# Kernel tuning notes

Hardware: AMD Instinct MI355X
Metric: run time of the kernel (lower is better)

Reference implementation:

```python
import jax, jax.numpy as jnp
import numpy as np

D = 1024
DK = 1024
B, S = 4, 2048

def setup_inputs() -> dict:
    key = jax.random.key(0)
    ks = jax.random.split(key, 7)
    x = jax.random.normal(ks[0], (B, S, D), dtype=jnp.float32)
    mask = jnp.zeros((B, S, S), dtype=jnp.float32)
    scale = 1.0 / np.sqrt(D)
    Wq = jax.random.normal(ks[1], (D, DK), dtype=jnp.float32) * scale
    bq = jax.random.normal(ks[2], (DK,), dtype=jnp.float32) * 0.01
    Wk = jax.random.normal(ks[3], (D, DK), dtype=jnp.float32) * scale
    bk = jax.random.normal(ks[4], (DK,), dtype=jnp.float32) * 0.01
    Wv = jax.random.normal(ks[5], (D, DK), dtype=jnp.float32) * scale
    bv = jax.random.normal(ks[6], (DK,), dtype=jnp.float32) * 0.01
    return {"x": x, "mask": mask, "Wq": Wq, "bq": bq, "Wk": Wk, "bk": bk, "Wv": Wv, "bv": bv}

def reference(x, mask, Wq, bq, Wk, bk, Wv, bv):
    # Q/K/V projections: [B,S,D] @ [D,DK] + bias -> [B,S,DK]
    Q = jnp.einsum('bsd,dk->bsk', x, Wq) + bq
    K = jnp.einsum('bsd,dk->bsk', x, Wk) + bk
    V = jnp.einsum('bsd,dk->bsk', x, Wv) + bv
    scale = 1.0 / jnp.sqrt(jnp.asarray(DK, dtype=Q.dtype))
    scores = jnp.einsum('bqk,bpk->bqp', Q, K) * scale + mask  # [B,S,S]
    attn = jax.nn.softmax(scores, axis=-1)
    return jnp.einsum('bqp,bpk->bqk', attn, V)
```

## Files before the change

### kernel.cpp

```cpp
#include <hip/hip_runtime.h>
#include <hip/hip_bf16.h>
#include <stdint.h>

typedef unsigned short u16;
typedef __attribute__((ext_vector_type(4))) unsigned short u16x4;
typedef __attribute__((ext_vector_type(8))) short short8;
typedef __attribute__((ext_vector_type(4))) float f32x4;

__device__ inline u16 f2b(float f) {
  uint32_t u = __builtin_bit_cast(uint32_t, f);
  u += 0x7fffu + ((u >> 16) & 1u);
  return (u16)(u >> 16);
}
__device__ inline float b2f(u16 b) {
  return __builtin_bit_cast(float, (uint32_t)b << 16);
}

__global__ __launch_bounds__(256) void cvt_f32_bf16(const float* __restrict__ in,
                                                    u16* __restrict__ out, long n) {
  long i = ((long)blockIdx.x * blockDim.x + threadIdx.x) * 4;
  if (i + 3 < n) {
    float4 v = *(const float4*)(in + i);
    u16x4 o = { f2b(v.x), f2b(v.y), f2b(v.z), f2b(v.w) };
    *(u16x4*)(out + i) = o;
  }
}

__global__ __launch_bounds__(256) void transpose_cvt3(const float* __restrict__ Wq,
                                                      const float* __restrict__ Wk,
                                                      const float* __restrict__ Wv,
                                                      u16* __restrict__ out) {
  const int z = blockIdx.z;
  const float* in = z == 0 ? Wq : (z == 1 ? Wk : Wv);
  u16* o = out + (long)z * 1024 * 1024;
  __shared__ float tile[32][33];
  int c0 = blockIdx.x * 32, r0 = blockIdx.y * 32;
#pragma unroll
  for (int j = 0; j < 32; j += 8)
    tile[threadIdx.y + j][threadIdx.x] = in[(long)(r0 + threadIdx.y + j) * 1024 + c0 + threadIdx.x];
  __syncthreads();
#pragma unroll
  for (int j = 0; j < 32; j += 8)
    o[(long)(c0 + threadIdx.y + j) * 1024 + r0 + threadIdx.x] = f2b(tile[threadIdx.x][threadIdx.y + j]);
}

__global__ __launch_bounds__(256) void concat_bias(const float* __restrict__ bq,
                                                   const float* __restrict__ bk,
                                                   const float* __restrict__ bv,
                                                   float* __restrict__ out) {
  int i = blockIdx.x * 256 + threadIdx.x;
  if (i < 3072)
    out[i] = i < 1024 ? bq[i] : (i < 2048 ? bk[i - 1024] : bv[i - 2048]);
}

#define BM 128
#define BN 128
#define BK 64

__device__ inline void load_lds16(const void* g, void* l) {
  __builtin_amdgcn_global_load_lds((const __attribute__((address_space(1))) void*)g,
                                   (__attribute__((address_space(3))) void*)l, 16, 0, 0);
}

__global__ __launch_bounds__(256, 2) void gemm_bt(
    const u16* __restrict__ A, const u16* __restrict__ Bt, void* __restrict__ C,
    u16* __restrict__ vtOut,
    const float* __restrict__ bias, const float* __restrict__ linv,
    int K, int lda, int ldb, int ldc,
    long sA, long sB, long sC,
    float scale, int mode)
{
  const int z = blockIdx.z;
  A += z * sA;
  Bt += z * sB;
  const long cbase = z * sC;
  const float* lz = linv ? linv + (long)z * 2048 : nullptr;

  __shared__ __align__(16) u16 lA[BM * BK];
  __shared__ __align__(16) u16 lB[BN * BK];

  const int t = threadIdx.x;
  const int lane = t & 63;
  const int wave = t >> 6;
  const int wr = wave >> 1, wc = wave & 1;
  const int m0 = blockIdx.y * BM, n0 = blockIdx.x * BN;

  const int srow = t >> 3;
  const int schunk = (t & 7) ^ (srow & 7);
  const u16* aS = A + (long)(m0 + srow) * lda + schunk * 8;
  const u16* bS = Bt + (long)(n0 + srow) * ldb + schunk * 8;

  f32x4 acc[4][4] = {};
  const int fr = lane & 15;
  const int q4 = lane >> 4;

  for (int k0 = 0; k0 < K; k0 += BK) {
    __syncthreads();
#pragma unroll
    for (int i = 0; i < 4; i++) {
      load_lds16(aS + k0 + (long)(i * 32) * lda, &lA[(i * 256 + t) * 8]);
      load_lds16(bS + k0 + (long)(i * 32) * ldb, &lB[(i * 256 + t) * 8]);
    }
    __syncthreads();
#pragma unroll
    for (int kk = 0; kk < 2; kk++) {
      const int ch = kk * 4 + q4;
      short8 aF[4], bF[4];
#pragma unroll
      for (int i = 0; i < 4; i++) {
        int row = wr * 64 + i * 16 + fr;
        aF[i] = *(const short8*)&lA[row * BK + ((ch ^ (row & 7)) * 8)];
      }
#pragma unroll
      for (int j = 0; j < 4; j++) {
        int row = wc * 64 + j * 16 + fr;
        bF[j] = *(const short8*)&lB[row * BK + ((ch ^ (row & 7)) * 8)];
      }
#pragma unroll
      for (int i = 0; i < 4; i++)
#pragma unroll
        for (int j = 0; j < 4; j++)
          acc[i][j] = __builtin_amdgcn_mfma_f32_16x16x32_bf16(aF[i], bF[j], acc[i][j], 0, 0, 0);
    }
  }

  const int r0 = q4 * 4;
#pragma unroll
  for (int i = 0; i < 4; i++) {
#pragma unroll
    for (int j = 0; j < 4; j++) {
      const int row = m0 + wr * 64 + i * 16 + r0;
      const int col = n0 + wc * 64 + j * 16 + fr;
      if (mode == 0) {
        const float b = bias[col];
        if (col >= 2048) {
          u16x4 o = { f2b(acc[i][j][0] + b), f2b(acc[i][j][1] + b),
                      f2b(acc[i][j][2] + b), f2b(acc[i][j][3] + b) };
          *(u16x4*)(vtOut + (long)(col - 2048) * 8192 + row) = o;
        } else {
#pragma unroll
          for (int r = 0; r < 4; r++)
            ((u16*)C)[(long)(row + r) * ldc + col] = f2b(acc[i][j][r] + b);
        }
      } else if (mode == 2) {
#pragma unroll
        for (int r = 0; r < 4; r++)
          ((u16*)C)[cbase + (long)(row + r) * ldc + col] = f2b(__expf(acc[i][j][r] * scale));
      } else {
#pragma unroll
        for (int r = 0; r < 4; r++)
          ((float*)C)[cbase + (long)(row + r) * ldc + col] = acc[i][j][r] * lz[row + r];
      }
    }
  }
}

__global__ __launch_bounds__(256) void maskexp_rows(u16* __restrict__ P,
                                                    const float* __restrict__ mask,
                                                    float* __restrict__ linv) {
  const long row = blockIdx.x;
  u16* p = P + row * 2048;
  const float* mk = mask + row * 2048;
  const int t = threadIdx.x;
  const int wave = t >> 6;

  u16x4 a0 = *(const u16x4*)(p + 8 * t);
  u16x4 a1 = *(const u16x4*)(p + 8 * t + 4);
  float4 m0 = *(const float4*)(mk + 8 * t);
  float4 m1 = *(const float4*)(mk + 8 * t + 4);

  float e[8];
  e[0] = b2f(a0.x) * __expf(m0.x); e[1] = b2f(a0.y) * __expf(m0.y);
  e[2] = b2f(a0.z) * __expf(m0.z); e[3] = b2f(a0.w) * __expf(m0.w);
  e[4] = b2f(a1.x) * __expf(m1.x); e[5] = b2f(a1.y) * __expf(m1.y);
  e[6] = b2f(a1.z) * __expf(m1.z); e[7] = b2f(a1.w) * __expf(m1.w);

  float sum = ((e[0] + e[1]) + (e[2] + e[3])) + ((e[4] + e[5]) + (e[6] + e[7]));
#pragma unroll
  for (int off = 32; off > 0; off >>= 1) sum += __shfl_xor(sum, off);
  __shared__ float reds[4];
  if ((t & 63) == 0) reds[wave] = sum;
  __syncthreads();
  sum = (reds[0] + reds[1]) + (reds[2] + reds[3]);
  if (t == 0) linv[row] = 1.0f / sum;

  u16x4 o0 = { f2b(e[0]), f2b(e[1]), f2b(e[2]), f2b(e[3]) };
  u16x4 o1 = { f2b(e[4]), f2b(e[5]), f2b(e[6]), f2b(e[7]) };
  *(u16x4*)(p + 8 * t) = o0;
  *(u16x4*)(p + 8 * t + 4) = o1;
}

extern "C" void kernel_launch(void* const* d_in, const int* in_sizes, int n_in,
                              void* d_out, int out_size, void* d_ws, size_t ws_size,
                              hipStream_t stream) {
  const float* x    = (const float*)d_in[0];
  const float* mask = (const float*)d_in[1];
  const float* Wq   = (const float*)d_in[2];
  const float* bq   = (const float*)d_in[3];
  const float* Wk   = (const float*)d_in[4];
  const float* bk   = (const float*)d_in[5];
  const float* Wv   = (const float*)d_in[6];
  const float* bv   = (const float*)d_in[7];
  float* out = (float*)d_out;

  char* w = (char*)d_ws;
  u16*   xb    = (u16*)(w);
  u16*   wT    = (u16*)(w + 16777216);
  float* biasC = (float*)(w + 23068672);
  u16*   QKV   = (u16*)(w + 23081088);
  u16*   Vt    = (u16*)(w + 73414016);
  u16*   Pp    = (u16*)(w + 90191232);
  float* linv  = (float*)(w + 123745664);

  cvt_f32_bf16<<<8192, 256, 0, stream>>>(x, xb, 8192L * 1024);
  transpose_cvt3<<<dim3(32, 32, 3), dim3(32, 8), 0, stream>>>(Wq, Wk, Wv, wT);
  concat_bias<<<12, 256, 0, stream>>>(bq, bk, bv, biasC);

  gemm_bt<<<dim3(24, 64, 1), 256, 0, stream>>>(xb, wT, QKV, Vt, biasC, nullptr,
      1024, 1024, 1024, 3072, 0, 0, 0, 1.0f, 0);

  gemm_bt<<<dim3(16, 16, 4), 256, 0, stream>>>(QKV, QKV + 1024, Pp, nullptr, nullptr, nullptr,
      1024, 3072, 3072, 2048,
      2048L * 3072, 2048L * 3072, 2048L * 2048, 0.03125f, 2);

  maskexp_rows<<<8192, 256, 0, stream>>>(Pp, mask, linv);

  gemm_bt<<<dim3(8, 16, 4), 256, 0, stream>>>(Pp, Vt, out, nullptr, nullptr, linv,
      2048, 2048, 8192, 1024,
      2048L * 2048, 2048L, 2048L * 1024, 1.0f, 4);
}
```

Before: 309.9 us.

## Fuse mask-exp and row-sum into the QK^T GEMM epilogue

Drops the separate maskexp_rows pass. The scores GEMM epilogue now stages exp(scores) through LDS, multiplies by exp(mask), writes P once with coalesced stores and accumulates partial row sums with atomicAdd into a zeroed buffer. The PV GEMM computes 1/rowsum itself. This removes a full read-modify-write of the 32MB P matrix. In exchange it adds atomics, an extra memset and a double rounding of exp to bf16.

```diff
diff --git a/kernel.cpp b/kernel.cpp
--- a/kernel.cpp
+++ b/kernel.cpp
@@ -65,7 +65,8 @@
 __global__ __launch_bounds__(256, 2) void gemm_bt(
     const u16* __restrict__ A, const u16* __restrict__ Bt, void* __restrict__ C,
     u16* __restrict__ vtOut,
-    const float* __restrict__ bias, const float* __restrict__ linv,
+    const float* __restrict__ bias,
+    const float* __restrict__ mask, float* __restrict__ rowsum,
     int K, int lda, int ldb, int ldc,
     long sA, long sB, long sC,
     float scale, int mode)
@@ -74,10 +75,10 @@
   A += z * sA;
   Bt += z * sB;
   const long cbase = z * sC;
-  const float* lz = linv ? linv + (long)z * 2048 : nullptr;
-
-  __shared__ __align__(16) u16 lA[BM * BK];
-  __shared__ __align__(16) u16 lB[BN * BK];
+
+  __shared__ __align__(16) u16 smem[2 * BM * BK];
+  u16* lA = smem;
+  u16* lB = smem + BM * BK;
 
   const int t = threadIdx.x;
   const int lane = t & 63;
@@ -125,8 +126,60 @@
   }
 
   const int r0 = q4 * 4;
+  if (mode == 2) {
+    __syncthreads();
+#pragma unroll
+    for (int i = 0; i < 4; i++)
+#pragma unroll
+      for (int j = 0; j < 4; j++) {
+        const int rl = wr * 64 + i * 16 + r0;
+        const int cl = wc * 64 + j * 16 + fr;
+        const int ch = cl >> 3, co = cl & 7;
+#pragma unroll
+        for (int r = 0; r < 4; r++)
+          smem[(rl + r) * 128 + (((ch ^ ((rl + r) & 15)) * 8) | co)] =
+              f2b(__expf(acc[i][j][r] * scale));
+      }
+    __syncthreads();
+    const int rl = t >> 1, half = t & 1;
+    const long mb = (long)z * 2048 * 2048;
+    const float* mrow = mask + mb + (long)(m0 + rl) * 2048 + n0 + half * 64;
+    u16* prow = (u16*)C + cbase + (long)(m0 + rl) * ldc + n0 + half * 64;
+    float sum = 0.0f;
+#pragma unroll
+    for (int k = 0; k < 8; k++) {
+      const int g = half * 8 + k;
+      short8 v8 = *(const short8*)&smem[rl * 128 + ((g ^ (rl & 15)) * 8)];
+      float4 mk0 = *(const float4*)(mrow + k * 8);
+      float4 mk1 = *(const float4*)(mrow + k * 8 + 4);
+      float e0 = b2f((u16)v8[0]) * __expf(mk0.x);
+      float e1 = b2f((u16)v8[1]) * __expf(mk0.y);
+      float e2 = b2f((u16)v8[2]) * __expf(mk0.z);
+      float e3 = b2f((u16)v8[3]) * __expf(mk0.w);
+      float e4 = b2f((u16)v8[4]) * __expf(mk1.x);
+      float e5 = b2f((u16)v8[5]) * __expf(mk1.y);
+      float e6 = b2f((u16)v8[6]) * __expf(mk1.z);
+      float e7 = b2f((u16)v8[7]) * __expf(mk1.w);
+      sum += ((e0 + e1) + (e2 + e3)) + ((e4 + e5) + (e6 + e7));
+      u16x4 o0 = { f2b(e0), f2b(e1), f2b(e2), f2b(e3) };
+      u16x4 o1 = { f2b(e4), f2b(e5), f2b(e6), f2b(e7) };
+      *(u16x4*)(prow + k * 8) = o0;
+      *(u16x4*)(prow + k * 8 + 4) = o1;
+    }
+    sum += __shfl_xor(sum, 1);
+    if (half == 0)
+      atomicAdd(&rowsum[(long)z * 2048 + m0 + rl], sum);
+    return;
+  }
+
 #pragma unroll
   for (int i = 0; i < 4; i++) {
+    float inv[4];
+    if (mode == 4) {
+      const int rowb = m0 + wr * 64 + i * 16 + r0;
+#pragma unroll
+      for (int r = 0; r < 4; r++) inv[r] = 1.0f / rowsum[(long)z * 2048 + rowb + r];
+    }
 #pragma unroll
     for (int j = 0; j < 4; j++) {
       const int row = m0 + wr * 64 + i * 16 + r0;
@@ -142,52 +195,13 @@
           for (int r = 0; r < 4; r++)
             ((u16*)C)[(long)(row + r) * ldc + col] = f2b(acc[i][j][r] + b);
         }
-      } else if (mode == 2) {
+      } else {
 #pragma unroll
         for (int r = 0; r < 4; r++)
-          ((u16*)C)[cbase + (long)(row + r) * ldc + col] = f2b(__expf(acc[i][j][r] * scale));
-      } else {
-#pragma unroll
-        for (int r = 0; r < 4; r++)
-          ((float*)C)[cbase + (long)(row + r) * ldc + col] = acc[i][j][r] * lz[row + r];
-      }
-    }
-  }
-}
-
-__global__ __launch_bounds__(256) void maskexp_rows(u16* __restrict__ P,
-                                                    const float* __restrict__ mask,
-                                                    float* __restrict__ linv) {
-  const long row = blockIdx.x;
-  u16* p = P + row * 2048;
-  const float* mk = mask + row * 2048;
-  const int t = threadIdx.x;
-  const int wave = t >> 6;
-
-  u16x4 a0 = *(const u16x4*)(p + 8 * t);
-  u16x4 a1 = *(const u16x4*)(p + 8 * t + 4);
-  float4 m0 = *(const float4*)(mk + 8 * t);
-  float4 m1 = *(const float4*)(mk + 8 * t + 4);
-
-  float e[8];
-  e[0] = b2f(a0.x) * __expf(m0.x); e[1] = b2f(a0.y) * __expf(m0.y);
-  e[2] = b2f(a0.z) * __expf(m0.z); e[3] = b2f(a0.w) * __expf(m0.w);
-  e[4] = b2f(a1.x) * __expf(m1.x); e[5] = b2f(a1.y) * __expf(m1.y);
-  e[6] = b2f(a1.z) * __expf(m1.z); e[7] = b2f(a1.w) * __expf(m1.w);
-
-  float sum = ((e[0] + e[1]) + (e[2] + e[3])) + ((e[4] + e[5]) + (e[6] + e[7]));
-#pragma unroll
-  for (int off = 32; off > 0; off >>= 1) sum += __shfl_xor(sum, off);
-  __shared__ float reds[4];
-  if ((t & 63) == 0) reds[wave] = sum;
-  __syncthreads();
-  sum = (reds[0] + reds[1]) + (reds[2] + reds[3]);
-  if (t == 0) linv[row] = 1.0f / sum;
-
-  u16x4 o0 = { f2b(e[0]), f2b(e[1]), f2b(e[2]), f2b(e[3]) };
-  u16x4 o1 = { f2b(e[4]), f2b(e[5]), f2b(e[6]), f2b(e[7]) };
-  *(u16x4*)(p + 8 * t) = o0;
-  *(u16x4*)(p + 8 * t + 4) = o1;
+          ((float*)C)[cbase + (long)(row + r) * ldc + col] = acc[i][j][r] * inv[r];
+      }
+    }
+  }
 }
 
 extern "C" void kernel_launch(void* const* d_in, const int* in_sizes, int n_in,
@@ -210,22 +224,23 @@
   u16*   QKV   = (u16*)(w + 23081088);
   u16*   Vt    = (u16*)(w + 73414016);
   u16*   Pp    = (u16*)(w + 90191232);
-  float* linv  = (float*)(w + 123745664);
+  float* rsum  = (float*)(w + 123745664);
 
   cvt_f32_bf16<<<8192, 256, 0, stream>>>(x, xb, 8192L * 1024);
   transpose_cvt3<<<dim3(32, 32, 3), dim3(32, 8), 0, stream>>>(Wq, Wk, Wv, wT);
   concat_bias<<<12, 256, 0, stream>>>(bq, bk, bv, biasC);
-
-  gemm_bt<<<dim3(24, 64, 1), 256, 0, stream>>>(xb, wT, QKV, Vt, biasC, nullptr,
+  hipMemsetAsync(rsum, 0, 8192 * sizeof(float), stream);
+
+  gemm_bt<<<dim3(24, 64, 1), 256, 0, stream>>>(xb, wT, QKV, Vt, biasC, nullptr, nullptr,
       1024, 1024, 1024, 3072, 0, 0, 0, 1.0f, 0);
 
-  gemm_bt<<<dim3(16, 16, 4), 256, 0, stream>>>(QKV, QKV + 1024, Pp, nullptr, nullptr, nullptr,
+  gemm_bt<<<dim3(16, 16, 4), 256, 0, stream>>>(QKV, QKV + 1024, Pp, nullptr, nullptr,
+      mask, rsum,
       1024, 3072, 3072, 2048,
       2048L * 3072, 2048L * 3072, 2048L * 2048, 0.03125f, 2);
 
-  maskexp_rows<<<8192, 256, 0, stream>>>(Pp, mask, linv);
-
-  gemm_bt<<<dim3(8, 16, 4), 256, 0, stream>>>(Pp, Vt, out, nullptr, nullptr, linv,
+  gemm_bt<<<dim3(8, 16, 4), 256, 0, stream>>>(Pp, Vt, out, nullptr, nullptr,
+      nullptr, rsum,
       2048, 2048, 8192, 1024,
       2048L * 2048, 2048L, 2048L * 1024, 1.0f, 4);
 }
```

Result: no change. 312.0 us (+0.7%).
